# Kernel tuning notes

Hardware: AMD Instinct MI355X
Metric: run time of the kernel (lower is better)

## Reference

```python
import jax, jax.numpy as jnp
import numpy as np

H = 4096          # hidden_size
M = 4096          # num tokens
BLK = 128         # fp8 quant group/block size
EPS = 1e-6
FP8_MAX = 448.0   # float8_e4m3fn max


def fp8_round(x):
    # round-trip through fp8 e4m3 to emulate FP8 storage
    return x.astype(jnp.float8_e4m3fn).astype(jnp.float32)


def rms_norm(x, w, eps=EPS):
    var = jnp.mean(x * x, axis=-1, keepdims=True)
    return x * jax.lax.rsqrt(var + eps) * w


def block_fp8_linear(x, w, wscale):
    # per-token group-128 activation quant + 128x128 block-scaled fp8 GEMM
    m, k = x.shape
    kb = k // BLK
    nb = w.shape[1] // BLK
    xr = x.reshape(m, kb, BLK)
    amax = jnp.max(jnp.abs(xr), axis=-1)                      # [m, kb]
    s = jnp.maximum(amax, 1e-12) / FP8_MAX                    # group scales
    q = fp8_round(xr / s[..., None])                          # fp8 values
    xdq = (q * s[..., None]).reshape(m, k)                    # dequant acts
    # dequantize weight blockwise: w already fp8-valued floats
    wdq = (w.reshape(kb, BLK, nb, BLK) * wscale[:, None, :, None]).reshape(k, nb * BLK)
    return xdq @ wdq


def setup_inputs() -> dict:
    key = jax.random.key(0)
    ks = jax.random.split(key, 8)
    x = jax.random.normal(ks[0], (M, H), dtype=jnp.float32)
    sb = H // BLK
    d = {"x": x}
    for i in range(3):
        w = fp8_round(jax.random.uniform(ks[1 + i], (H, H), dtype=jnp.float32)).T
        d[f"w{i}"] = w
        d[f"ws{i}"] = jax.random.uniform(ks[4 + i], (sb, sb), dtype=jnp.float32)
    for i in range(4):
        d[f"nw{i}"] = jnp.ones((H,), dtype=jnp.float32)
    return d


def reference(x, w0, ws0, w1, ws1, w2, ws2, nw0, nw1, nw2, nw3):
    x = jax.nn.relu(x)
    resid = x
    y = rms_norm(x, nw0)
    x2 = block_fp8_linear(y, w0, ws0)
    resid = x2 + resid
    y2 = rms_norm(resid, nw1)
    x3 = block_fp8_linear(y2, w1, ws1)
    resid = x3 + resid
    y3 = rms_norm(resid, nw2)
    x4 = block_fp8_linear(y3, w2, ws2)
    resid = x4 + resid
    y4 = rms_norm(resid, nw3)
    return y4
```

## Files before the change

### kernel.cpp

```cpp
#include <hip/hip_runtime.h>
#include <stdint.h>

#define H 4096

typedef float v4f __attribute__((ext_vector_type(4)));
typedef long long i64;
typedef long long v2l __attribute__((ext_vector_type(2)));

__device__ __forceinline__ void gload16(const uint8_t* g, uint8_t* l) {
  __builtin_amdgcn_global_load_lds(
      (const __attribute__((address_space(1))) uint8_t*)g,
      (__attribute__((address_space(3))) uint8_t*)l, 16, 0, 0);
}

__device__ __forceinline__ int permpos(int kg) {
  const int kb = kg >> 7, b = kg & 127;
  const int ks = b >> 5, q = (b >> 3) & 3, j = b & 7;
  return kb * 128 + q * 32 + ks * 8 + j;
}

__global__ __launch_bounds__(256) void conv_w_kernel(
    const float* __restrict__ w0, const float* __restrict__ w1,
    const float* __restrict__ w2, uint8_t* __restrict__ o0,
    uint8_t* __restrict__ o1, uint8_t* __restrict__ o2) {
  const float* w = (blockIdx.z == 0) ? w0 : (blockIdx.z == 1 ? w1 : w2);
  uint8_t* o = (blockIdx.z == 0) ? o0 : (blockIdx.z == 1 ? o1 : o2);
  __shared__ uint8_t t[64][68];
  const int tid = threadIdx.x;
  const int k0 = blockIdx.y * 64, n0 = blockIdx.x * 64;
  const int rr = tid >> 4, cc = (tid & 15) * 4;
#pragma unroll
  for (int j = 0; j < 4; ++j) {
    const int r = rr + j * 16;
    v4f f = *(const v4f*)(w + (size_t)(k0 + r) * H + n0 + cc);
    unsigned p = __builtin_amdgcn_cvt_pk_fp8_f32(f.x, f.y, 0, false);
    p = __builtin_amdgcn_cvt_pk_fp8_f32(f.z, f.w, p, true);
    t[cc + 0][r] = p & 0xff;
    t[cc + 1][r] = (p >> 8) & 0xff;
    t[cc + 2][r] = (p >> 16) & 0xff;
    t[cc + 3][r] = p >> 24;
  }
  __syncthreads();
#pragma unroll
  for (int j = 0; j < 4; ++j) {
    const int n = rr + j * 16;
    unsigned p = (unsigned)t[n][cc] | ((unsigned)t[n][cc + 1] << 8) |
                 ((unsigned)t[n][cc + 2] << 16) |
                 ((unsigned)t[n][cc + 3] << 24);
    *(unsigned*)(o + (size_t)(n0 + n) * H + permpos(k0 + cc)) = p;
  }
}

__global__ __launch_bounds__(256) void quant_kernel(
    const float* in, const float* __restrict__ nw, uint8_t* __restrict__ q,
    float* __restrict__ sxT, const int relu) {
  const int row = blockIdx.x, tid = threadIdx.x;
  const v4f* rp = (const v4f*)(in + (size_t)row * H);
  v4f v[4];
  float ss = 0.f;
#pragma unroll
  for (int j = 0; j < 4; ++j) {
    v4f x = rp[j * 256 + tid];
    if (relu) {
      x.x = fmaxf(x.x, 0.f); x.y = fmaxf(x.y, 0.f);
      x.z = fmaxf(x.z, 0.f); x.w = fmaxf(x.w, 0.f);
    }
    v[j] = x;
    ss += x.x * x.x + x.y * x.y + x.z * x.z + x.w * x.w;
  }
#pragma unroll
  for (int o = 32; o > 0; o >>= 1) ss += __shfl_down(ss, o);
  __shared__ float red[4];
  if ((tid & 63) == 0) red[tid >> 6] = ss;
  __syncthreads();
  ss = red[0] + red[1] + red[2] + red[3];
  const float rinv = 1.f / sqrtf(ss * (1.f / H) + 1e-6f);
#pragma unroll
  for (int j = 0; j < 4; ++j) {
    v4f nv = ((const v4f*)nw)[j * 256 + tid];
    v4f y;
    y.x = v[j].x * rinv * nv.x;
    y.y = v[j].y * rinv * nv.y;
    y.z = v[j].z * rinv * nv.z;
    y.w = v[j].w * rinv * nv.w;
    float am = fmaxf(fmaxf(fabsf(y.x), fabsf(y.y)), fmaxf(fabsf(y.z), fabsf(y.w)));
#pragma unroll
    for (int o = 16; o > 0; o >>= 1) am = fmaxf(am, __shfl_xor(am, o, 32));
    const float s = fmaxf(am, 1e-12f) / 448.f;
    unsigned p = __builtin_amdgcn_cvt_pk_fp8_f32(y.x / s, y.y / s, 0, false);
    p = __builtin_amdgcn_cvt_pk_fp8_f32(y.z / s, y.w / s, p, true);
    const int col = (j * 256 + tid) * 4;
    *(unsigned*)(q + (size_t)row * H + permpos(col)) = p;
    if ((tid & 31) == 0)
      sxT[(size_t)(j * 8 + (tid >> 5)) * 4096 + row] = s;
  }
}

__global__ __launch_bounds__(256) void norm_kernel(float* io,
                                                   const float* __restrict__ nw) {
  const int row = blockIdx.x, tid = threadIdx.x;
  v4f* rp = (v4f*)(io + (size_t)row * H);
  v4f v[4];
  float ss = 0.f;
#pragma unroll
  for (int j = 0; j < 4; ++j) {
    v4f x = rp[j * 256 + tid];
    v[j] = x;
    ss += x.x * x.x + x.y * x.y + x.z * x.z + x.w * x.w;
  }
#pragma unroll
  for (int o = 32; o > 0; o >>= 1) ss += __shfl_down(ss, o);
  __shared__ float red[4];
  if ((tid & 63) == 0) red[tid >> 6] = ss;
  __syncthreads();
  ss = red[0] + red[1] + red[2] + red[3];
  const float rinv = 1.f / sqrtf(ss * (1.f / H) + 1e-6f);
#pragma unroll
  for (int j = 0; j < 4; ++j) {
    v4f nv = ((const v4f*)nw)[j * 256 + tid];
    v4f y;
    y.x = v[j].x * rinv * nv.x;
    y.y = v[j].y * rinv * nv.y;
    y.z = v[j].z * rinv * nv.z;
    y.w = v[j].w * rinv * nv.w;
    rp[j * 256 + tid] = y;
  }
}

__global__ __launch_bounds__(512, 2) void gemm_kernel(
    const uint8_t* __restrict__ qa,
    const float* __restrict__ sxT,
    const uint8_t* __restrict__ wt,
    const float* __restrict__ ws,
    const float* resid, float* outp, const int relu) {
  __shared__ __attribute__((aligned(16))) uint8_t sA[2][32768];
  __shared__ __attribute__((aligned(16))) uint8_t sB[2][32768];
  __shared__ __attribute__((aligned(16))) float scb[2][256];
  __shared__ float ws_s[64];

  const int tid = threadIdx.x;

  const int lid = blockIdx.y * 16 + blockIdx.x;
  const int nl = (lid & 7) * 32 + (lid >> 3);
  const int m0 = (nl >> 4) * 256, n0 = (nl & 15) * 256;

  const int w = tid >> 6, lane = tid & 63;
  const int quad = lane >> 4, l16 = lane & 15;
  const int wm = w >> 2, wn = w & 3;
  const int whalf = wn >> 1;

  if (tid < 64) ws_s[tid] = ws[(tid >> 1) * 32 + (n0 >> 7) + (tid & 1)];

  const int sw = (tid & 7) ^ ((tid >> 3) & 7);
  const uint8_t* gA = qa + (size_t)(m0 + (tid >> 3)) * H + sw * 16;
  const uint8_t* gB = wt + (size_t)(n0 + (tid >> 3)) * H + sw * 16;
  const uint8_t* gS = (const uint8_t*)sxT + (size_t)m0 * 4 + lane * 16;
  const int ldst = w * 1024;

#pragma unroll
  for (int i = 0; i < 4; ++i) {
    gload16(gA + (size_t)i * (64 * H), sA[0] + i * 8192 + ldst);
    gload16(gB + (size_t)i * (64 * H), sB[0] + i * 8192 + ldst);
  }
  if (w == 0) gload16(gS, (uint8_t*)scb[0]);

  int offp[2];
#pragma unroll
  for (int ksp = 0; ksp < 2; ++ksp)
    offp[ksp] = (((quad * 2 + ksp) ^ (l16 & 7)) << 4);

  const v4f zf = {0.f, 0.f, 0.f, 0.f};
  v4f acc[8][4];
#pragma unroll
  for (int i = 0; i < 8; ++i)
#pragma unroll
    for (int j = 0; j < 4; ++j) acc[i][j] = zf;

  __syncthreads();

  for (int kb = 0; kb < 32; ++kb) {
    const int cur = kb & 1, nxt = cur ^ 1;
    const uint8_t* Ab = sA[cur];
    const uint8_t* Bb = sB[cur];
    const float* sc = scb[cur];
    const float wsk = ws_s[kb * 2 + whalf];
    const bool pf = (kb < 31);
    v2l bf[4][2];

#pragma unroll
    for (int p = 0; p < 4; ++p) {
      if (p == 0) {
#pragma unroll
        for (int tc = 0; tc < 4; ++tc)
#pragma unroll
          for (int ksp = 0; ksp < 2; ++ksp)
            bf[tc][ksp] =
                *(const v2l*)(Bb + (wn * 64 + tc * 16 + l16) * 128 + offp[ksp]);
      }
      v2l a[2][2];
      v4f s4[2];
#pragma unroll
      for (int t = 0; t < 2; ++t) {
        const int row = wm * 128 + (p * 2 + t) * 16 + l16;
        a[t][0] = *(const v2l*)(Ab + row * 128 + offp[0]);
        a[t][1] = *(const v2l*)(Ab + row * 128 + offp[1]);
        s4[t] = *(const v4f*)(sc + wm * 128 + (p * 2 + t) * 16 + quad * 4);
      }
      if (pf) {
        gload16(gA + 128 + (size_t)p * (64 * H), sA[nxt] + p * 8192 + ldst);
        gload16(gB + 128 + (size_t)p * (64 * H), sB[nxt] + p * 8192 + ldst);
        if (p == 0 && w == 0) gload16(gS + 16384, (uint8_t*)scb[nxt]);
      }
      __builtin_amdgcn_s_barrier();
      asm volatile("s_waitcnt lgkmcnt(0)" ::: "memory");
      __builtin_amdgcn_sched_barrier(0);
      __builtin_amdgcn_s_setprio(1);
#pragma unroll
      for (int t = 0; t < 2; ++t) {
        const int tr = p * 2 + t;
        const v4f sv = s4[t] * wsk;
#pragma unroll
        for (int tc = 0; tc < 4; ++tc) {
          v4f pr = __builtin_amdgcn_mfma_f32_16x16x32_fp8_fp8(a[t][0].x, bf[tc][0].x, zf, 0, 0, 0);
          pr = __builtin_amdgcn_mfma_f32_16x16x32_fp8_fp8(a[t][0].y, bf[tc][0].y, pr, 0, 0, 0);
          pr = __builtin_amdgcn_mfma_f32_16x16x32_fp8_fp8(a[t][1].x, bf[tc][1].x, pr, 0, 0, 0);
          pr = __builtin_amdgcn_mfma_f32_16x16x32_fp8_fp8(a[t][1].y, bf[tc][1].y, pr, 0, 0, 0);
          acc[tr][tc] += pr * sv;
        }
      }
      __builtin_amdgcn_s_setprio(0);
      if (p == 3) asm volatile("s_waitcnt vmcnt(0)" ::: "memory");
      __builtin_amdgcn_s_barrier();
    }
    gA += 128;
    gB += 128;
    gS += 16384;
  }

  const int mB = m0 + wm * 128 + quad * 4;
  const int nB = n0 + wn * 64 + l16;
#pragma unroll
  for (int tr = 0; tr < 8; ++tr) {
#pragma unroll
    for (int r = 0; r < 4; ++r) {
      const size_t rowOff = (size_t)(mB + tr * 16 + r) * H;
#pragma unroll
      for (int tc = 0; tc < 4; ++tc) {
        const size_t idx = rowOff + nB + tc * 16;
        float rv = resid[idx];
        if (relu) rv = fmaxf(rv, 0.f);
        outp[idx] = acc[tr][tc][r] + rv;
      }
    }
  }
}

extern "C" void kernel_launch(void* const* d_in, const int* in_sizes, int n_in,
                              void* d_out, int out_size, void* d_ws, size_t ws_size,
                              hipStream_t stream) {
  const float* x   = (const float*)d_in[0];
  const float* w0  = (const float*)d_in[1];
  const float* ws0 = (const float*)d_in[2];
  const float* w1  = (const float*)d_in[3];
  const float* ws1 = (const float*)d_in[4];
  const float* w2  = (const float*)d_in[5];
  const float* ws2 = (const float*)d_in[6];
  const float* nw0 = (const float*)d_in[7];
  const float* nw1 = (const float*)d_in[8];
  const float* nw2 = (const float*)d_in[9];
  const float* nw3 = (const float*)d_in[10];
  float* R = (float*)d_out;

  uint8_t* base = (uint8_t*)d_ws;
  uint8_t* wq0 = base;
  uint8_t* wq1 = base + ((size_t)16 << 20);
  uint8_t* wq2 = base + ((size_t)32 << 20);
  uint8_t* qa  = base + ((size_t)48 << 20);
  float* sa    = (float*)(base + ((size_t)64 << 20));

  conv_w_kernel<<<dim3(64, 64, 3), 256, 0, stream>>>(w0, w1, w2, wq0, wq1, wq2);

  quant_kernel<<<4096, 256, 0, stream>>>(x, nw0, qa, sa, 1);
  gemm_kernel<<<dim3(16, 16), 512, 0, stream>>>(qa, sa, wq0, ws0, x, R, 1);

  quant_kernel<<<4096, 256, 0, stream>>>(R, nw1, qa, sa, 0);
  gemm_kernel<<<dim3(16, 16), 512, 0, stream>>>(qa, sa, wq1, ws1, R, R, 0);

  quant_kernel<<<4096, 256, 0, stream>>>(R, nw2, qa, sa, 0);
  gemm_kernel<<<dim3(16, 16), 512, 0, stream>>>(qa, sa, wq2, ws2, R, R, 0);

  norm_kernel<<<4096, 256, 0, stream>>>(R, nw3);
}
```

Baseline: 771.2 us.

## Deepen GEMM LDS pipeline to four half-K stages with counted vmcnt waits

Splits each 128-wide K block into two 64-byte half stages and cycles them through a four-slot LDS ring buffer (same total LDS), prefetching three stages ahead. It replaces the per-block drain with s_waitcnt vmcnt(15), so several global-to-LDS loads stay in flight while the MFMAs run. It also changes the global load mapping and the LDS swizzle to 32-byte chunks per lane. The intent is to hide global memory latency better, at the cost of more barriers per K block and fragile hand-counted waits.

```diff
diff --git a/kernel.cpp b/kernel.cpp
--- a/kernel.cpp
+++ b/kernel.cpp
@@ -133,9 +133,9 @@
     const uint8_t* __restrict__ wt,
     const float* __restrict__ ws,
     const float* resid, float* outp, const int relu) {
-  __shared__ __attribute__((aligned(16))) uint8_t sA[2][32768];
-  __shared__ __attribute__((aligned(16))) uint8_t sB[2][32768];
-  __shared__ __attribute__((aligned(16))) float scb[2][256];
+  __shared__ __attribute__((aligned(16))) uint8_t sA[4][16384];
+  __shared__ __attribute__((aligned(16))) uint8_t sB[4][16384];
+  __shared__ __attribute__((aligned(16))) float scb[4][256];
   __shared__ float ws_s[64];
 
   const int tid = threadIdx.x;
@@ -144,30 +144,35 @@
   const int nl = (lid & 7) * 32 + (lid >> 3);
   const int m0 = (nl >> 4) * 256, n0 = (nl & 15) * 256;
 
-  const int w = tid >> 6, lane = tid & 63;
+  const int wv = tid >> 6, lane = tid & 63;
   const int quad = lane >> 4, l16 = lane & 15;
-  const int wm = w >> 2, wn = w & 3;
+  const int wm = wv >> 2, wn = wv & 3;
   const int whalf = wn >> 1;
 
   if (tid < 64) ws_s[tid] = ws[(tid >> 1) * 32 + (n0 >> 7) + (tid & 1)];
 
-  const int sw = (tid & 7) ^ ((tid >> 3) & 7);
-  const uint8_t* gA = qa + (size_t)(m0 + (tid >> 3)) * H + sw * 16;
-  const uint8_t* gB = wt + (size_t)(n0 + (tid >> 3)) * H + sw * 16;
-  const uint8_t* gS = (const uint8_t*)sxT + (size_t)m0 * 4 + lane * 16;
-  const int ldst = w * 1024;
-
-#pragma unroll
-  for (int i = 0; i < 4; ++i) {
-    gload16(gA + (size_t)i * (64 * H), sA[0] + i * 8192 + ldst);
-    gload16(gB + (size_t)i * (64 * H), sB[0] + i * 8192 + ldst);
-  }
-  if (w == 0) gload16(gS, (uint8_t*)scb[0]);
-
-  int offp[2];
-#pragma unroll
-  for (int ksp = 0; ksp < 2; ++ksp)
-    offp[ksp] = (((quad * 2 + ksp) ^ (l16 & 7)) << 4);
+  const int lr = lane >> 2;
+  const int qch = (lane & 3) ^ ((lane >> 3) & 3);
+  const uint8_t* pAg = qa + (size_t)(m0 + wv * 32 + lr) * H + qch * 32;
+  const uint8_t* pBg = wt + (size_t)(n0 + wv * 32 + lr) * H + qch * 32;
+  const uint8_t* pSg = (const uint8_t*)sxT + (size_t)m0 * 4 + lane * 16;
+
+  auto stage = [&](int j) {
+    const int kb_ = j >> 1, par_ = j & 1, bi_ = j & 3;
+    const size_t ko_ = (size_t)kb_ * 128 + par_ * 16;
+    gload16(pAg + ko_, sA[bi_] + wv * 2048);
+    gload16(pAg + (size_t)16 * H + ko_, sA[bi_] + wv * 2048 + 1024);
+    gload16(pBg + ko_, sB[bi_] + wv * 2048);
+    gload16(pBg + (size_t)16 * H + ko_, sB[bi_] + wv * 2048 + 1024);
+    int kbs_ = (j + 2) >> 1;
+    if (kbs_ > 31) kbs_ = 31;
+    gload16(pSg + (size_t)kbs_ * 16384, (uint8_t*)scb[kbs_ & 3]);
+  };
+
+  const int swq = (quad ^ ((l16 >> 1) & 3)) << 4;
+  const int aoff = (wm * 128 + l16) * 64 + swq;
+  const int boff = (wn * 64 + l16) * 64 + swq;
+  const int soff = wm * 512 + quad * 16;
 
   const v4f zf = {0.f, 0.f, 0.f, 0.f};
   v4f acc[8][4];
@@ -176,66 +181,55 @@
 #pragma unroll
     for (int j = 0; j < 4; ++j) acc[i][j] = zf;
 
-  __syncthreads();
-
-  for (int kb = 0; kb < 32; ++kb) {
-    const int cur = kb & 1, nxt = cur ^ 1;
-    const uint8_t* Ab = sA[cur];
-    const uint8_t* Bb = sB[cur];
-    const float* sc = scb[cur];
-    const float wsk = ws_s[kb * 2 + whalf];
-    const bool pf = (kb < 31);
-    v2l bf[4][2];
-
-#pragma unroll
-    for (int p = 0; p < 4; ++p) {
-      if (p == 0) {
-#pragma unroll
-        for (int tc = 0; tc < 4; ++tc)
-#pragma unroll
-          for (int ksp = 0; ksp < 2; ++ksp)
-            bf[tc][ksp] =
-                *(const v2l*)(Bb + (wn * 64 + tc * 16 + l16) * 128 + offp[ksp]);
+  gload16(pSg, (uint8_t*)scb[0]);
+  stage(0);
+  stage(1);
+  stage(2);
+  __syncthreads();
+
+  auto dostep = [&](int ks) {
+    __builtin_amdgcn_s_barrier();
+    __builtin_amdgcn_sched_barrier(0);
+    const uint8_t* Ab = sA[ks & 3];
+    const uint8_t* Bb = sB[ks & 3];
+    const uint8_t* Sb = (const uint8_t*)scb[(ks >> 1) & 3];
+    const float wsk = ws_s[(ks >> 1) * 2 + whalf];
+    v2l b[4], a[8];
+    v4f s4[8];
+#pragma unroll
+    for (int tc = 0; tc < 4; ++tc) b[tc] = *(const v2l*)(Bb + boff + tc * 1024);
+#pragma unroll
+    for (int tr = 0; tr < 8; ++tr) a[tr] = *(const v2l*)(Ab + aoff + tr * 1024);
+#pragma unroll
+    for (int tr = 0; tr < 8; ++tr) s4[tr] = *(const v4f*)(Sb + soff + tr * 64);
+    asm volatile("s_waitcnt lgkmcnt(0)" ::: "memory");
+    __builtin_amdgcn_sched_barrier(0);
+    __builtin_amdgcn_s_setprio(1);
+#pragma unroll
+    for (int tr = 0; tr < 8; ++tr) {
+      const v4f sv = s4[tr] * wsk;
+#pragma unroll
+      for (int tc = 0; tc < 4; ++tc) {
+        v4f pr = __builtin_amdgcn_mfma_f32_16x16x32_fp8_fp8(a[tr].x, b[tc].x, zf, 0, 0, 0);
+        pr = __builtin_amdgcn_mfma_f32_16x16x32_fp8_fp8(a[tr].y, b[tc].y, pr, 0, 0, 0);
+        acc[tr][tc] += pr * sv;
       }
-      v2l a[2][2];
-      v4f s4[2];
-#pragma unroll
-      for (int t = 0; t < 2; ++t) {
-        const int row = wm * 128 + (p * 2 + t) * 16 + l16;
-        a[t][0] = *(const v2l*)(Ab + row * 128 + offp[0]);
-        a[t][1] = *(const v2l*)(Ab + row * 128 + offp[1]);
-        s4[t] = *(const v4f*)(sc + wm * 128 + (p * 2 + t) * 16 + quad * 4);
-      }
-      if (pf) {
-        gload16(gA + 128 + (size_t)p * (64 * H), sA[nxt] + p * 8192 + ldst);
-        gload16(gB + 128 + (size_t)p * (64 * H), sB[nxt] + p * 8192 + ldst);
-        if (p == 0 && w == 0) gload16(gS + 16384, (uint8_t*)scb[nxt]);
-      }
-      __builtin_amdgcn_s_barrier();
-      asm volatile("s_waitcnt lgkmcnt(0)" ::: "memory");
-      __builtin_amdgcn_sched_barrier(0);
-      __builtin_amdgcn_s_setprio(1);
-#pragma unroll
-      for (int t = 0; t < 2; ++t) {
-        const int tr = p * 2 + t;
-        const v4f sv = s4[t] * wsk;
-#pragma unroll
-        for (int tc = 0; tc < 4; ++tc) {
-          v4f pr = __builtin_amdgcn_mfma_f32_16x16x32_fp8_fp8(a[t][0].x, bf[tc][0].x, zf, 0, 0, 0);
-          pr = __builtin_amdgcn_mfma_f32_16x16x32_fp8_fp8(a[t][0].y, bf[tc][0].y, pr, 0, 0, 0);
-          pr = __builtin_amdgcn_mfma_f32_16x16x32_fp8_fp8(a[t][1].x, bf[tc][1].x, pr, 0, 0, 0);
-          pr = __builtin_amdgcn_mfma_f32_16x16x32_fp8_fp8(a[t][1].y, bf[tc][1].y, pr, 0, 0, 0);
-          acc[tr][tc] += pr * sv;
-        }
-      }
-      __builtin_amdgcn_s_setprio(0);
-      if (p == 3) asm volatile("s_waitcnt vmcnt(0)" ::: "memory");
-      __builtin_amdgcn_s_barrier();
     }
-    gA += 128;
-    gB += 128;
-    gS += 16384;
-  }
+    __builtin_amdgcn_s_setprio(0);
+    __builtin_amdgcn_s_barrier();
+  };
+
+  for (int ks = 0; ks < 61; ++ks) {
+    stage(ks + 3);
+    asm volatile("s_waitcnt vmcnt(15)" ::: "memory");
+    dostep(ks);
+  }
+  asm volatile("s_waitcnt vmcnt(10)" ::: "memory");
+  dostep(61);
+  asm volatile("s_waitcnt vmcnt(5)" ::: "memory");
+  dostep(62);
+  asm volatile("s_waitcnt vmcnt(0)" ::: "memory");
+  dostep(63);
 
   const int mB = m0 + wm * 128 + quad * 4;
   const int nB = n0 + wn * 64 + l16;
```

After: 869.6 us. 12.8% more time.
